# Kernel optimization log

Measured on AMD Instinct MI355X. Metric: run time of the kernel, lower is better.

## Reference

```python
import jax, jax.numpy as jnp
import numpy as np

DIM = 384
NUM_HEADS = 12
WS = 8            # window_size
SS = 4            # shift_size
HEAD_DIM = DIM // NUM_HEADS
SCALE = HEAD_DIM ** -0.5
N = WS * WS       # tokens per window
EPS = 1e-5
MLP_HIDDEN = 4 * DIM

# relative position index (static, matches torch buffer construction)
_coords = np.stack(np.meshgrid(np.arange(WS), np.arange(WS), indexing='ij')).reshape(2, -1)
_rel = (_coords[:, :, None] - _coords[:, None, :]).transpose(1, 2, 0)  # [N,N,2]
_rel[..., 0] += WS - 1
_rel[..., 1] += WS - 1
_rel[..., 0] *= 2 * WS - 1
RPI = jnp.asarray(_rel.sum(-1))  # [N,N] int


def layer_norm(x, g, b):
    m = x.mean(-1, keepdims=True)
    v = ((x - m) ** 2).mean(-1, keepdims=True)
    return (x - m) / jnp.sqrt(v + EPS) * g + b


def window_partition(x):
    B, Hh, Ww, C = x.shape
    x = x.reshape(B, Hh // WS, WS, Ww // WS, WS, C).transpose(0, 1, 3, 2, 4, 5)
    return x.reshape(-1, WS, WS, C)


def window_reverse(w, Hh, Ww):
    B = w.shape[0] // ((Hh // WS) * (Ww // WS))
    x = w.reshape(B, Hh // WS, Ww // WS, WS, WS, -1).transpose(0, 1, 3, 2, 4, 5)
    return x.reshape(B, Hh, Ww, -1)


def attention_mask(Hp, Wp):
    # region id along each axis: 0 = [0, Hp-WS), 1 = [Hp-WS, Hp-SS), 2 = [Hp-SS, Hp)
    h_id = np.zeros(Hp, np.int32); h_id[Hp - WS:Hp - SS] = 1; h_id[Hp - SS:] = 2
    w_id = np.zeros(Wp, np.int32); w_id[Wp - WS:Wp - SS] = 1; w_id[Wp - SS:] = 2
    cnt = h_id[:, None] * 3 + w_id[None, :]                      # [Hp, Wp]
    img = jnp.asarray(cnt, jnp.float32).reshape(1, Hp, Wp, 1)
    mw = window_partition(img).reshape(-1, N)                    # [nW, N]
    am = mw[:, None, :] - mw[:, :, None]                         # [nW, N, N]
    return jnp.where(am != 0, jnp.float32(-100.0), jnp.float32(0.0))


def setup_inputs() -> dict:
    key = jax.random.key(0)
    ks = jax.random.split(key, 8)
    B, H, W = 32, 64, 64
    std = 0.02
    return {
        'x': jax.random.normal(ks[0], (B, H * W, DIM), jnp.float32),
        'qkv_w': jax.random.normal(ks[1], (DIM, 3 * DIM), jnp.float32) * std,
        'qkv_b': jnp.zeros((3 * DIM,), jnp.float32),
        'proj_w': jax.random.normal(ks[2], (DIM, DIM), jnp.float32) * std,
        'proj_b': jnp.zeros((DIM,), jnp.float32),
        'rpb_table': jax.random.normal(ks[3], ((2 * WS - 1) * (2 * WS - 1), NUM_HEADS), jnp.float32) * std,
        'n1_g': jnp.ones((DIM,), jnp.float32), 'n1_b': jnp.zeros((DIM,), jnp.float32),
        'n2_g': jnp.ones((DIM,), jnp.float32), 'n2_b': jnp.zeros((DIM,), jnp.float32),
        'fc1_w': jax.random.normal(ks[4], (DIM, MLP_HIDDEN), jnp.float32) * std,
        'fc1_b': jnp.zeros((MLP_HIDDEN,), jnp.float32),
        'fc2_w': jax.random.normal(ks[5], (MLP_HIDDEN, DIM), jnp.float32) * std,
        'fc2_b': jnp.zeros((DIM,), jnp.float32),
        'H': 64, 'W': 64,
    }


def reference(x, qkv_w, qkv_b, proj_w, proj_b, rpb_table, n1_g, n1_b, n2_g, n2_b,
              fc1_w, fc1_b, fc2_w, fc2_b, H, W):
    B, L, C = x.shape
    shortcut = x
    h = layer_norm(x, n1_g, n1_b).reshape(B, H, W, C)
    pad_r = (WS - W % WS) % WS
    pad_b = (WS - H % WS) % WS
    if pad_r or pad_b:
        h = jnp.pad(h, ((0, 0), (0, pad_b), (0, pad_r), (0, 0)))
    Hp, Wp = H + pad_b, W + pad_r
    shifted = jnp.roll(h, shift=(-SS, -SS), axis=(1, 2))
    xw = window_partition(shifted).reshape(-1, N, C)             # [B_, N, C]
    B_ = xw.shape[0]

    qkv = (xw @ qkv_w + qkv_b).reshape(B_, N, 3, NUM_HEADS, HEAD_DIM)
    q = qkv[:, :, 0].transpose(0, 2, 1, 3) * SCALE               # [B_, h, N, d]
    k = qkv[:, :, 1].transpose(0, 2, 1, 3)
    v = qkv[:, :, 2].transpose(0, 2, 1, 3)

    attn = jnp.einsum('bhnd,bhmd->bhnm', q, k)                   # [B_, h, N, N]
    bias = rpb_table[RPI].transpose(2, 0, 1)                     # [h, N, N]
    attn = attn + bias[None]

    mask = attention_mask(Hp, Wp)                                # [nW, N, N]
    nW = mask.shape[0]
    attn = attn.reshape(B_ // nW, nW, NUM_HEADS, N, N) + mask[None, :, None]
    attn = jax.nn.softmax(attn.reshape(B_, NUM_HEADS, N, N), axis=-1)

    out = jnp.einsum('bhnm,bhmd->bhnd', attn, v)
    out = out.transpose(0, 2, 1, 3).reshape(B_, N, C)
    out = out @ proj_w + proj_b

    out = window_reverse(out.reshape(-1, WS, WS, C), Hp, Wp)
    out = jnp.roll(out, shift=(SS, SS), axis=(1, 2))
    out = out[:, :H, :W, :].reshape(B, H * W, C)

    x = shortcut + out
    h2 = layer_norm(x, n2_g, n2_b)
    mlp = jax.nn.gelu(h2 @ fc1_w + fc1_b, approximate=False) @ fc2_w + fc2_b
    return x + mlp
```

## Files before the change

### kernel.cpp

```cpp
#include <hip/hip_runtime.h>
#include <math.h>


#define ROWS_TOTAL 131072
#define NWIN_TOTAL 2048

typedef __attribute__((ext_vector_type(8))) __bf16 bf16x8;
typedef __attribute__((ext_vector_type(4))) float f32x4;
typedef __attribute__((ext_vector_type(8))) unsigned short ushort8;

__device__ __forceinline__ unsigned short f2bf(float f) {
  unsigned u = __builtin_bit_cast(unsigned, f);
  u = (u + 0x7fffu + ((u >> 16) & 1u)) >> 16;
  return (unsigned short)u;
}
__device__ __forceinline__ float bf2f(unsigned short u) {
  return __builtin_bit_cast(float, (unsigned)u << 16);
}

__device__ __forceinline__ void gload16(const void* g, void* l) {
  __builtin_amdgcn_global_load_lds(
      (const __attribute__((address_space(1))) unsigned int*)g,
      (__attribute__((address_space(3))) unsigned int*)l, 16, 0, 0);
}

__device__ __forceinline__ int gather_row(int win, int t) {
  int b = win >> 6, wi = (win >> 3) & 7, wj = win & 7;
  int gi = (wi * 8 + (t >> 3) + 4) & 63;
  int gj = (wj * 8 + (t & 7) + 4) & 63;
  return (b << 12) + (gi << 6) + gj;
}

__device__ __forceinline__ float gelu_f(float v) {
  float x = v * 0.70710678118654752f;
  float ax = fabsf(x);
  float t = 1.f / (1.f + 0.3275911f * ax);
  float poly =
      t * (0.254829592f +
           t * (-0.284496736f +
                t * (1.421413741f + t * (-1.453152027f + t * 1.061405429f))));
  float er = 1.f - poly * __expf(-x * x);
  er = copysignf(er, x);
  return 0.5f * v * (1.f + er);
}

#define STG(buf_, t_)                                                   \
  {                                                                     \
    size_t ko = (size_t)(t_) * 64;                                      \
    gload16(aS0 + ko, (char*)As + (buf_) * 8192 + tid * 16);            \
    gload16(aS1 + ko, (char*)As + (buf_) * 8192 + 4096 + tid * 16);     \
    gload16(bS0 + ko, (char*)Bs + (buf_) * 6144 + tid * 16);            \
    if (tid < 128)                                                      \
      gload16(bS1 + ko, (char*)Bs + (buf_) * 6144 + 4096 + tid * 16);   \
  }

#define GEMM_DECLS()                                                    \
  f32x4 acc[4][3];                                                      \
  _Pragma("unroll") for (int i_ = 0; i_ < 4; ++i_)                      \
  _Pragma("unroll") for (int j_ = 0; j_ < 3; ++j_)                      \
      acc[i_][j_] = (f32x4)(0.f);                                       \
  int aO[4], bO[3];                                                     \
  _Pragma("unroll") for (int mi_ = 0; mi_ < 4; ++mi_)                   \
      aO[mi_] = (wr * 64 + mi_ * 16 + lr) * 32 + hi * 8;                \
  _Pragma("unroll") for (int nj_ = 0; nj_ < 3; ++nj_)                   \
      bO[nj_] = (wc * 48 + nj_ * 16 + lr) * 32 + hi * 8;

#define GEMM_CORE(NT_)                                                  \
  {                                                                     \
    int cur = 0;                                                        \
    STG(0, 0);                                                          \
    __syncthreads();                                                    \
    for (int t = 0; t < (NT_); ++t) {                                   \
      if (t + 1 < (NT_)) STG(cur ^ 1, t + 1);                           \
      const ushort* AsC = &As[cur][0];                                  \
      const ushort* BsC = &Bs[cur][0];                                  \
      bf16x8 bv[3];                                                     \
      _Pragma("unroll") for (int nj = 0; nj < 3; ++nj)                  \
          bv[nj] = *(const bf16x8*)(BsC + bO[nj]);                      \
      _Pragma("unroll") for (int mi = 0; mi < 4; ++mi) {                \
        bf16x8 av = *(const bf16x8*)(AsC + aO[mi]);                     \
        _Pragma("unroll") for (int nj = 0; nj < 3; ++nj)                \
          acc[mi][nj] = __builtin_amdgcn_mfma_f32_16x16x32_bf16(        \
              av, bv[nj], acc[mi][nj], 0, 0, 0);                        \
      }                                                                 \
      __syncthreads();                                                  \
      cur ^= 1;                                                         \
    }                                                                   \
  }

#define GRID_SWZ(NP_)                                                   \
  int p, bm;                                                            \
  {                                                                     \
    int lin = blockIdx.y * (NP_) + blockIdx.x;                          \
    if ((gridDim.y & 7) == 0) {                                         \
      int xcd = lin & 7, q = lin >> 3;                                  \
      p = q % (NP_); bm = (q / (NP_)) * 8 + xcd;                        \
    } else { p = blockIdx.x; bm = blockIdx.y; }                         \
  }

__global__ __launch_bounds__(256) void wprep_k(
    const float* __restrict__ qkvw, const float* __restrict__ projw,
    const float* __restrict__ fc1w, const float* __restrict__ fc2w,
    ushort* __restrict__ wq, ushort* __restrict__ wp,
    ushort* __restrict__ w1, ushort* __restrict__ w2) {
  int gid = blockIdx.x * 256 + threadIdx.x;
  const int S1 = 1152 * 384;
  const int S2 = S1 + 384 * 384;
  const int S3 = S2 + 1536 * 384;
  const int S4 = S3 + 384 * 1536;
  if (gid < S1) {
    int n = gid / 384, k = gid - n * 384;
    wq[gid] = f2bf(qkvw[(size_t)k * 1152 + n]);
  } else if (gid < S2) {
    int i = gid - S1, n = i / 384, k = i - n * 384;
    wp[i] = f2bf(projw[(size_t)k * 384 + n]);
  } else if (gid < S3) {
    int i = gid - S2, n = i / 384, k = i - n * 384;
    w1[i] = f2bf(fc1w[(size_t)k * 1536 + n]);
  } else if (gid < S4) {
    int i = gid - S3, n = i / 1536, k = i - n * 1536;
    w2[i] = f2bf(fc2w[(size_t)k * 384 + n]);
  }
}

__global__ __launch_bounds__(256) void ln_fused_k(
    const float* __restrict__ x, const float* __restrict__ g,
    const float* __restrict__ b, ushort* __restrict__ o) {
  int wid = threadIdx.x >> 6, lane = threadIdx.x & 63;
  int row = (blockIdx.x << 2) + wid;
  const float* p = x + (size_t)row * 384;
  float2 v[3];
  float s = 0.f, ss = 0.f;
#pragma unroll
  for (int c = 0; c < 3; ++c) {
    v[c] = *(const float2*)(p + lane * 2 + c * 128);
    s += v[c].x + v[c].y;
    ss += v[c].x * v[c].x + v[c].y * v[c].y;
  }
#pragma unroll
  for (int off = 1; off < 64; off <<= 1) {
    s += __shfl_xor(s, off);
    ss += __shfl_xor(ss, off);
  }
  float m = s * (1.f / 384.f);
  float r = rsqrtf(ss * (1.f / 384.f) - m * m + 1e-5f);
  ushort* op = o + (size_t)row * 384;
#pragma unroll
  for (int c = 0; c < 3; ++c) {
    float2 gg = *(const float2*)(g + lane * 2 + c * 128);
    float2 bb = *(const float2*)(b + lane * 2 + c * 128);
    union { ushort u[2]; unsigned w; } pk;
    pk.u[0] = f2bf((v[c].x - m) * r * gg.x + bb.x);
    pk.u[1] = f2bf((v[c].y - m) * r * gg.y + bb.y);
    *(unsigned*)(op + lane * 2 + c * 128) = pk.w;
  }
}

__global__ __launch_bounds__(256) void qkv_mfma_k(
    const ushort* __restrict__ xln, const ushort* __restrict__ wq,
    const float* __restrict__ qkvb, ushort* __restrict__ qkvd, int wc0) {
  __shared__ __align__(16) ushort As[2][4096];
  __shared__ __align__(16) ushort Bs[2][3072];
  const int tid = threadIdx.x;
  const int lane = tid & 63;
  const int w = tid >> 6;
  const int wr = w >> 1, wc = w & 1;
  const int lr = lane & 15, hi = lane >> 4;
  GRID_SWZ(12);
  const int n0 = p * 96;
  int r0 = tid >> 2, r1 = (256 + tid) >> 2;
  const char* aS0 = (const char*)xln +
                    (size_t)gather_row(wc0 + bm * 2 + (r0 >> 6), r0 & 63) * 768 +
                    (tid & 3) * 16;
  const char* aS1 = (const char*)xln +
                    (size_t)gather_row(wc0 + bm * 2 + (r1 >> 6), r1 & 63) * 768 +
                    ((256 + tid) & 3) * 16;
  const char* bS0 = (const char*)wq + (size_t)(n0 + (tid >> 2)) * 768 +
                    (tid & 3) * 16;
  const char* bS1 = (const char*)wq + (size_t)(n0 + 64 + (tid >> 2)) * 768 +
                    (tid & 3) * 16;
  GEMM_DECLS();
  GEMM_CORE(12);
  const float scale = 0.17677669529663687f;
#pragma unroll
  for (int mi = 0; mi < 4; ++mi) {
#pragma unroll
    for (int r = 0; r < 4; ++r) {
      int rr = wr * 64 + mi * 16 + (hi << 2) + r;
      size_t row = (size_t)(bm * 128 + rr);
#pragma unroll
      for (int nj = 0; nj < 3; ++nj) {
        int nc = n0 + wc * 48 + nj * 16 + lr;
        float v = acc[mi][nj][r] + qkvb[nc];
        if (nc < 384) v *= scale;
        qkvd[row * 1152 + nc] = f2bf(v);
      }
    }
  }
}

__global__ __launch_bounds__(128) void attn_k(
    const ushort* __restrict__ qkv, const float* __restrict__ rpb,
    ushort* __restrict__ ao, int wc0) {
  __shared__ __align__(16) float kbuf[2][64][32];
  __shared__ __align__(16) float vbuf[2][64][32];
  __shared__ float bias[2][232];
  __shared__ int region[64];
  const int tid = threadIdx.x;
  const int wid = tid >> 6, lane = tid & 63;
  const int w = blockIdx.x, win = wc0 + w;
  const int head = blockIdx.y * 2 + wid;
  if (tid < 64) {
    int wi = (win >> 3) & 7, wj = win & 7;
    int pi = wi * 8 + (tid >> 3), pj = wj * 8 + (tid & 7);
    int ri = pi < 56 ? 0 : (pi < 60 ? 1 : 2);
    int rj = pj < 56 ? 0 : (pj < 60 ? 1 : 2);
    region[tid] = ri * 3 + rj;
  }
  const ushort* base = qkv + (size_t)(w * 64) * 1152;
  const int kcol = 384 + head * 32, vcol = 768 + head * 32;
#pragma unroll
  for (int s = 0; s < 4; ++s) {
    int f = s * 64 + lane;
    int r = f >> 2, c = (f & 3) * 8;
    ushort8 ku = *(const ushort8*)(base + (size_t)r * 1152 + kcol + c);
    ushort8 vu = *(const ushort8*)(base + (size_t)r * 1152 + vcol + c);
#pragma unroll
    for (int j = 0; j < 8; ++j) {
      kbuf[wid][r][c + j] = bf2f(ku[j]);
      vbuf[wid][r][c + j] = bf2f(vu[j]);
    }
  }
  for (int s = lane; s < 225; s += 64) bias[wid][s] = rpb[s * 12 + head];
  __syncthreads();
  const int i = lane;
  float qr[32];
  const ushort* qp = base + (size_t)i * 1152 + head * 32;
#pragma unroll
  for (int c = 0; c < 4; ++c) {
    ushort8 qu = *(const ushort8*)(qp + c * 8);
#pragma unroll
    for (int j = 0; j < 8; ++j) qr[c * 8 + j] = bf2f(qu[j]);
  }
  const int yi = i >> 3, xi = i & 7, regi = region[i];
  float sc[64];
  float mx = -3.0e38f;
#pragma unroll
  for (int j = 0; j < 64; ++j) {
    float a = 0.f;
#pragma unroll
    for (int c = 0; c < 32; c += 4) {
      float4 kv = *(float4*)&kbuf[wid][j][c];
      a = fmaf(qr[c], kv.x, a);
      a = fmaf(qr[c + 1], kv.y, a);
      a = fmaf(qr[c + 2], kv.z, a);
      a = fmaf(qr[c + 3], kv.w, a);
    }
    int dy = yi - (j >> 3) + 7, dx = xi - (j & 7) + 7;
    a += bias[wid][dy * 15 + dx];
    if (region[j] != regi) a -= 100.f;
    sc[j] = a;
    mx = fmaxf(mx, a);
  }
  float sum = 0.f;
#pragma unroll
  for (int j = 0; j < 64; ++j) {
    float e = __expf(sc[j] - mx);
    sc[j] = e;
    sum += e;
  }
  const float inv = 1.f / sum;
  float o[32];
#pragma unroll
  for (int c = 0; c < 32; ++c) o[c] = 0.f;
#pragma unroll
  for (int j = 0; j < 64; ++j) {
    float p = sc[j];
#pragma unroll
    for (int c = 0; c < 32; c += 4) {
      float4 vv = *(float4*)&vbuf[wid][j][c];
      o[c] = fmaf(p, vv.x, o[c]);
      o[c + 1] = fmaf(p, vv.y, o[c + 1]);
      o[c + 2] = fmaf(p, vv.z, o[c + 2]);
      o[c + 3] = fmaf(p, vv.w, o[c + 3]);
    }
  }
  ushort* op = ao + ((size_t)(w * 64 + i)) * 384 + (head << 5);
#pragma unroll
  for (int c = 0; c < 32; c += 8) {
    ushort8 pk;
#pragma unroll
    for (int j2 = 0; j2 < 8; ++j2) pk[j2] = f2bf(o[c + j2] * inv);
    *(ushort8*)(op + c) = pk;
  }
}

__global__ __launch_bounds__(256) void proj_mfma_k(
    const ushort* __restrict__ ao, const ushort* __restrict__ wp,
    const float* __restrict__ pb, const float* __restrict__ x,
    float* __restrict__ x2, int wc0) {
  __shared__ __align__(16) ushort As[2][4096];
  __shared__ __align__(16) ushort Bs[2][3072];
  const int tid = threadIdx.x;
  const int lane = tid & 63;
  const int w = tid >> 6;
  const int wr = w >> 1, wc = w & 1;
  const int lr = lane & 15, hi = lane >> 4;
  GRID_SWZ(4);
  const int n0 = p * 96;
  const char* aS0 = (const char*)ao +
                    (size_t)(bm * 128 + (tid >> 2)) * 768 + (tid & 3) * 16;
  const char* aS1 = (const char*)ao +
                    (size_t)(bm * 128 + 64 + (tid >> 2)) * 768 + (tid & 3) * 16;
  const char* bS0 = (const char*)wp + (size_t)(n0 + (tid >> 2)) * 768 +
                    (tid & 3) * 16;
  const char* bS1 = (const char*)wp + (size_t)(n0 + 64 + (tid >> 2)) * 768 +
                    (tid & 3) * 16;
  GEMM_DECLS();
  GEMM_CORE(12);
#pragma unroll
  for (int mi = 0; mi < 4; ++mi) {
#pragma unroll
    for (int r = 0; r < 4; ++r) {
      int rr = wr * 64 + mi * 16 + (hi << 2) + r;
      int gl = bm * 128 + rr;
      int gr = gather_row(wc0 + (gl >> 6), gl & 63);
#pragma unroll
      for (int nj = 0; nj < 3; ++nj) {
        int nc = n0 + wc * 48 + nj * 16 + lr;
        size_t idx = (size_t)gr * 384 + nc;
        x2[idx] = acc[mi][nj][r] + pb[nc] + x[idx];
      }
    }
  }
}

__global__ __launch_bounds__(256) void fc1_mfma_k(
    const ushort* __restrict__ x2ln, const ushort* __restrict__ w1,
    const float* __restrict__ fb, ushort* __restrict__ hm, int row0) {
  __shared__ __align__(16) ushort As[2][4096];
  __shared__ __align__(16) ushort Bs[2][3072];
  const int tid = threadIdx.x;
  const int lane = tid & 63;
  const int w = tid >> 6;
  const int wr = w >> 1, wc = w & 1;
  const int lr = lane & 15, hi = lane >> 4;
  GRID_SWZ(16);
  const int n0 = p * 96;
  const char* aS0 = (const char*)x2ln +
                    (size_t)(row0 + bm * 128 + (tid >> 2)) * 768 +
                    (tid & 3) * 16;
  const char* aS1 = (const char*)x2ln +
                    (size_t)(row0 + bm * 128 + 64 + (tid >> 2)) * 768 +
                    (tid & 3) * 16;
  const char* bS0 = (const char*)w1 + (size_t)(n0 + (tid >> 2)) * 768 +
                    (tid & 3) * 16;
  const char* bS1 = (const char*)w1 + (size_t)(n0 + 64 + (tid >> 2)) * 768 +
                    (tid & 3) * 16;
  GEMM_DECLS();
  GEMM_CORE(12);
#pragma unroll
  for (int mi = 0; mi < 4; ++mi) {
#pragma unroll
    for (int r = 0; r < 4; ++r) {
      int rr = wr * 64 + mi * 16 + (hi << 2) + r;
      size_t lrow = (size_t)(bm * 128 + rr);
#pragma unroll
      for (int nj = 0; nj < 3; ++nj) {
        int nc = n0 + wc * 48 + nj * 16 + lr;
        float v = gelu_f(acc[mi][nj][r] + fb[nc]);
        hm[lrow * 1536 + nc] = f2bf(v);
      }
    }
  }
}

__global__ __launch_bounds__(256) void fc2_mfma_k(
    const ushort* __restrict__ hm, const ushort* __restrict__ w2,
    const float* __restrict__ fb, float* __restrict__ out, int row0) {
  __shared__ __align__(16) ushort As[2][4096];
  __shared__ __align__(16) ushort Bs[2][3072];
  const int tid = threadIdx.x;
  const int lane = tid & 63;
  const int w = tid >> 6;
  const int wr = w >> 1, wc = w & 1;
  const int lr = lane & 15, hi = lane >> 4;
  GRID_SWZ(4);
  const int n0 = p * 96;
  const char* aS0 = (const char*)hm +
                    (size_t)(bm * 128 + (tid >> 2)) * 3072 + (tid & 3) * 16;
  const char* aS1 = (const char*)hm +
                    (size_t)(bm * 128 + 64 + (tid >> 2)) * 3072 +
                    (tid & 3) * 16;
  const char* bS0 = (const char*)w2 + (size_t)(n0 + (tid >> 2)) * 3072 +
                    (tid & 3) * 16;
  const char* bS1 = (const char*)w2 + (size_t)(n0 + 64 + (tid >> 2)) * 3072 +
                    (tid & 3) * 16;
  GEMM_DECLS();
  GEMM_CORE(48);
#pragma unroll
  for (int mi = 0; mi < 4; ++mi) {
#pragma unroll
    for (int r = 0; r < 4; ++r) {
      int rr = wr * 64 + mi * 16 + (hi << 2) + r;
      size_t grow = (size_t)(row0 + bm * 128 + rr);
#pragma unroll
      for (int nj = 0; nj < 3; ++nj) {
        int nc = n0 + wc * 48 + nj * 16 + lr;
        size_t idx = grow * 384 + nc;
        out[idx] = out[idx] + acc[mi][nj][r] + fb[nc];
      }
    }
  }
}

extern "C" void kernel_launch(void* const* d_in, const int* in_sizes, int n_in,
                              void* d_out, int out_size, void* d_ws, size_t ws_size,
                              hipStream_t stream) {
  const float* x = (const float*)d_in[0];
  const float* qkv_w = (const float*)d_in[1];
  const float* qkv_b = (const float*)d_in[2];
  const float* proj_w = (const float*)d_in[3];
  const float* proj_b = (const float*)d_in[4];
  const float* rpb = (const float*)d_in[5];
  const float* n1g = (const float*)d_in[6];
  const float* n1b = (const float*)d_in[7];
  const float* n2g = (const float*)d_in[8];
  const float* n2b = (const float*)d_in[9];
  const float* fc1w = (const float*)d_in[10];
  const float* fc1b = (const float*)d_in[11];
  const float* fc2w = (const float*)d_in[12];
  const float* fc2b = (const float*)d_in[13];
  float* out = (float*)d_out;
  char* ws = (char*)d_ws;

  ushort* wq = (ushort*)ws;
  ushort* wp = wq + 442368;
  ushort* w1 = wp + 147456;
  ushort* w2 = w1 + 589824;
  ushort* xln = (ushort*)(ws + 3538944);
  char* scratch = ws + 3538944 + 100663296;
  size_t base = 3538944 + 100663296;
  size_t ssz = (ws_size > base) ? ws_size - base : 0;

  wprep_k<<<6912, 256, 0, stream>>>(qkv_w, proj_w, fc1w, fc2w, wq, wp, w1, w2);
  ln_fused_k<<<ROWS_TOTAL / 4, 256, 0, stream>>>(x, n1g, n1b, xln);

  const size_t perwin = 196608;
  int nwc = (int)(ssz / perwin);
  if (nwc > NWIN_TOTAL) nwc = NWIN_TOTAL;
  nwc &= ~31;
  if (nwc < 32) nwc = 32;
  ushort* qkvd = (ushort*)scratch;
  ushort* ao = qkvd + (size_t)nwc * 73728;
  for (int wc0 = 0; wc0 < NWIN_TOTAL; wc0 += nwc) {
    int nw = (NWIN_TOTAL - wc0 < nwc) ? (NWIN_TOTAL - wc0) : nwc;
    qkv_mfma_k<<<dim3(12, nw / 2), 256, 0, stream>>>(xln, wq, qkv_b, qkvd,
                                                     wc0);
    attn_k<<<dim3(nw, 6), 128, 0, stream>>>(qkvd, rpb, ao, wc0);
    proj_mfma_k<<<dim3(4, nw / 2), 256, 0, stream>>>(ao, wp, proj_b, x, out,
                                                     wc0);
  }

  ln_fused_k<<<ROWS_TOTAL / 4, 256, 0, stream>>>(out, n2g, n2b, xln);
  const size_t pergrp = 393216;
  int ngc = (int)(ssz / pergrp);
  if (ngc > 1024) ngc = 1024;
  ngc &= ~7;
  if (ngc < 8) ngc = 8;
  ushort* hm = (ushort*)scratch;
  for (int g0 = 0; g0 < 1024; g0 += ngc) {
    int ng = (1024 - g0 < ngc) ? (1024 - g0) : ngc;
    fc1_mfma_k<<<dim3(16, ng), 256, 0, stream>>>(xln, w1, fc1b, hm, g0 * 128);
    fc2_mfma_k<<<dim3(4, ng), 256, 0, stream>>>(hm, w2, fc2b, out, g0 * 128);
  }
}
```

Measured before the change: 1.548 ms.

## Swizzle GEMM LDS tiles and store Q/K/V in per-head contiguous layout

Adds an XOR-style rotation of the 16-byte chunk positions, applied both to the global source offsets of the direct-to-LDS loads and to the LDS read offsets in all MFMA GEMMs. The goal is to remove LDS bank conflicts on the bf16x8 fragment reads. Separately, the QKV GEMM epilogue now writes Q, K and V into separate per-window, per-head contiguous buffers. This lets the attention kernel read its K/V/Q rows with contiguous 64-byte accesses instead of strided 2304-byte rows. The cost is scattered, less coalesced stores in the QKV epilogue.

Measured after the change: 1.552 ms. Within noise of the previous version (+0.2%).

```diff
diff --git a/kernel.cpp b/kernel.cpp
--- a/kernel.cpp
+++ b/kernel.cpp
@@ -60,10 +60,14 @@
   _Pragma("unroll") for (int j_ = 0; j_ < 3; ++j_)                      \
       acc[i_][j_] = (f32x4)(0.f);                                       \
   int aO[4], bO[3];                                                     \
-  _Pragma("unroll") for (int mi_ = 0; mi_ < 4; ++mi_)                   \
-      aO[mi_] = (wr * 64 + mi_ * 16 + lr) * 32 + hi * 8;                \
-  _Pragma("unroll") for (int nj_ = 0; nj_ < 3; ++nj_)                   \
-      bO[nj_] = (wc * 48 + nj_ * 16 + lr) * 32 + hi * 8;
+  _Pragma("unroll") for (int mi_ = 0; mi_ < 4; ++mi_) {                 \
+    int row_ = wr * 64 + mi_ * 16 + lr;                                 \
+    aO[mi_] = row_ * 32 + (((hi + (row_ >> 1)) & 3) << 3);              \
+  }                                                                     \
+  _Pragma("unroll") for (int nj_ = 0; nj_ < 3; ++nj_) {                 \
+    int row_ = wc * 48 + nj_ * 16 + lr;                                 \
+    bO[nj_] = row_ * 32 + (((hi + (row_ >> 1)) & 3) << 3);              \
+  }
 
 #define GEMM_CORE(NT_)                                                  \
   {                                                                     \
@@ -97,6 +101,8 @@
       p = q % (NP_); bm = (q / (NP_)) * 8 + xcd;                        \
     } else { p = blockIdx.x; bm = blockIdx.y; }                         \
   }
+
+#define SRC_SWZ(t_) (((((t_) & 3) - (((t_) >> 3) & 3)) & 3) << 4)
 
 __global__ __launch_bounds__(256) void wprep_k(
     const float* __restrict__ qkvw, const float* __restrict__ projw,
@@ -158,7 +164,8 @@
 
 __global__ __launch_bounds__(256) void qkv_mfma_k(
     const ushort* __restrict__ xln, const ushort* __restrict__ wq,
-    const float* __restrict__ qkvb, ushort* __restrict__ qkvd, int wc0) {
+    const float* __restrict__ qkvb, ushort* __restrict__ qd,
+    ushort* __restrict__ kd, ushort* __restrict__ vd, int wc0) {
   __shared__ __align__(16) ushort As[2][4096];
   __shared__ __align__(16) ushort Bs[2][3072];
   const int tid = threadIdx.x;
@@ -171,14 +178,14 @@
   int r0 = tid >> 2, r1 = (256 + tid) >> 2;
   const char* aS0 = (const char*)xln +
                     (size_t)gather_row(wc0 + bm * 2 + (r0 >> 6), r0 & 63) * 768 +
-                    (tid & 3) * 16;
+                    SRC_SWZ(tid);
   const char* aS1 = (const char*)xln +
                     (size_t)gather_row(wc0 + bm * 2 + (r1 >> 6), r1 & 63) * 768 +
-                    ((256 + tid) & 3) * 16;
+                    SRC_SWZ(tid);
   const char* bS0 = (const char*)wq + (size_t)(n0 + (tid >> 2)) * 768 +
-                    (tid & 3) * 16;
+                    SRC_SWZ(tid);
   const char* bS1 = (const char*)wq + (size_t)(n0 + 64 + (tid >> 2)) * 768 +
-                    (tid & 3) * 16;
+                    SRC_SWZ(tid);
   GEMM_DECLS();
   GEMM_CORE(12);
   const float scale = 0.17677669529663687f;
@@ -187,20 +194,24 @@
 #pragma unroll
     for (int r = 0; r < 4; ++r) {
       int rr = wr * 64 + mi * 16 + (hi << 2) + r;
-      size_t row = (size_t)(bm * 128 + rr);
+      int w_rel = bm * 2 + (rr >> 6), t = rr & 63;
 #pragma unroll
       for (int nj = 0; nj < 3; ++nj) {
         int nc = n0 + wc * 48 + nj * 16 + lr;
         float v = acc[mi][nj][r] + qkvb[nc];
-        if (nc < 384) v *= scale;
-        qkvd[row * 1152 + nc] = f2bf(v);
+        int qi = nc / 384, rem = nc - qi * 384;
+        int hh = rem >> 5, d = rem & 31;
+        ushort* base = (qi == 0) ? qd : (qi == 1 ? kd : vd);
+        if (qi == 0) v *= scale;
+        base[(((size_t)w_rel * 12 + hh) << 11) + (t << 5) + d] = f2bf(v);
       }
     }
   }
 }
 
 __global__ __launch_bounds__(128) void attn_k(
-    const ushort* __restrict__ qkv, const float* __restrict__ rpb,
+    const ushort* __restrict__ q, const ushort* __restrict__ k,
+    const ushort* __restrict__ v, const float* __restrict__ rpb,
     ushort* __restrict__ ao, int wc0) {
   __shared__ __align__(16) float kbuf[2][64][32];
   __shared__ __align__(16) float vbuf[2][64][32];
@@ -217,14 +228,15 @@
     int rj = pj < 56 ? 0 : (pj < 60 ? 1 : 2);
     region[tid] = ri * 3 + rj;
   }
-  const ushort* base = qkv + (size_t)(w * 64) * 1152;
-  const int kcol = 384 + head * 32, vcol = 768 + head * 32;
+  const size_t hb = ((size_t)w * 12 + head) * 2048;
+  const ushort* kp = k + hb;
+  const ushort* vp = v + hb;
 #pragma unroll
   for (int s = 0; s < 4; ++s) {
     int f = s * 64 + lane;
     int r = f >> 2, c = (f & 3) * 8;
-    ushort8 ku = *(const ushort8*)(base + (size_t)r * 1152 + kcol + c);
-    ushort8 vu = *(const ushort8*)(base + (size_t)r * 1152 + vcol + c);
+    ushort8 ku = *(const ushort8*)(kp + r * 32 + c);
+    ushort8 vu = *(const ushort8*)(vp + r * 32 + c);
 #pragma unroll
     for (int j = 0; j < 8; ++j) {
       kbuf[wid][r][c + j] = bf2f(ku[j]);
@@ -235,7 +247,7 @@
   __syncthreads();
   const int i = lane;
   float qr[32];
-  const ushort* qp = base + (size_t)i * 1152 + head * 32;
+  const ushort* qp = q + hb + (i << 5);
 #pragma unroll
   for (int c = 0; c < 4; ++c) {
     ushort8 qu = *(const ushort8*)(qp + c * 8);
@@ -309,13 +321,13 @@
   GRID_SWZ(4);
   const int n0 = p * 96;
   const char* aS0 = (const char*)ao +
-                    (size_t)(bm * 128 + (tid >> 2)) * 768 + (tid & 3) * 16;
+                    (size_t)(bm * 128 + (tid >> 2)) * 768 + SRC_SWZ(tid);
   const char* aS1 = (const char*)ao +
-                    (size_t)(bm * 128 + 64 + (tid >> 2)) * 768 + (tid & 3) * 16;
+                    (size_t)(bm * 128 + 64 + (tid >> 2)) * 768 + SRC_SWZ(tid);
   const char* bS0 = (const char*)wp + (size_t)(n0 + (tid >> 2)) * 768 +
-                    (tid & 3) * 16;
+                    SRC_SWZ(tid);
   const char* bS1 = (const char*)wp + (size_t)(n0 + 64 + (tid >> 2)) * 768 +
-                    (tid & 3) * 16;
+                    SRC_SWZ(tid);
   GEMM_DECLS();
   GEMM_CORE(12);
 #pragma unroll
@@ -349,14 +361,14 @@
   const int n0 = p * 96;
   const char* aS0 = (const char*)x2ln +
                     (size_t)(row0 + bm * 128 + (tid >> 2)) * 768 +
-                    (tid & 3) * 16;
+                    SRC_SWZ(tid);
   const char* aS1 = (const char*)x2ln +
                     (size_t)(row0 + bm * 128 + 64 + (tid >> 2)) * 768 +
-                    (tid & 3) * 16;
+                    SRC_SWZ(tid);
   const char* bS0 = (const char*)w1 + (size_t)(n0 + (tid >> 2)) * 768 +
-                    (tid & 3) * 16;
+                    SRC_SWZ(tid);
   const char* bS1 = (const char*)w1 + (size_t)(n0 + 64 + (tid >> 2)) * 768 +
-                    (tid & 3) * 16;
+                    SRC_SWZ(tid);
   GEMM_DECLS();
   GEMM_CORE(12);
 #pragma unroll
@@ -388,14 +400,14 @@
   GRID_SWZ(4);
   const int n0 = p * 96;
   const char* aS0 = (const char*)hm +
-                    (size_t)(bm * 128 + (tid >> 2)) * 3072 + (tid & 3) * 16;
+                    (size_t)(bm * 128 + (tid >> 2)) * 3072 + SRC_SWZ(tid);
   const char* aS1 = (const char*)hm +
                     (size_t)(bm * 128 + 64 + (tid >> 2)) * 3072 +
-                    (tid & 3) * 16;
+                    SRC_SWZ(tid);
   const char* bS0 = (const char*)w2 + (size_t)(n0 + (tid >> 2)) * 3072 +
-                    (tid & 3) * 16;
+                    SRC_SWZ(tid);
   const char* bS1 = (const char*)w2 + (size_t)(n0 + 64 + (tid >> 2)) * 3072 +
-                    (tid & 3) * 16;
+                    SRC_SWZ(tid);
   GEMM_DECLS();
   GEMM_CORE(48);
 #pragma unroll
@@ -451,13 +463,15 @@
   if (nwc > NWIN_TOTAL) nwc = NWIN_TOTAL;
   nwc &= ~31;
   if (nwc < 32) nwc = 32;
-  ushort* qkvd = (ushort*)scratch;
-  ushort* ao = qkvd + (size_t)nwc * 73728;
+  ushort* qd = (ushort*)scratch;
+  ushort* kd = qd + (size_t)nwc * 24576;
+  ushort* vd = kd + (size_t)nwc * 24576;
+  ushort* ao = vd + (size_t)nwc * 24576;
   for (int wc0 = 0; wc0 < NWIN_TOTAL; wc0 += nwc) {
     int nw = (NWIN_TOTAL - wc0 < nwc) ? (NWIN_TOTAL - wc0) : nwc;
-    qkv_mfma_k<<<dim3(12, nw / 2), 256, 0, stream>>>(xln, wq, qkv_b, qkvd,
-                                                     wc0);
-    attn_k<<<dim3(nw, 6), 128, 0, stream>>>(qkvd, rpb, ao, wc0);
+    qkv_mfma_k<<<dim3(12, nw / 2), 256, 0, stream>>>(xln, wq, qkv_b, qd, kd,
+                                                     vd, wc0);
+    attn_k<<<dim3(nw, 6), 128, 0, stream>>>(qd, kd, vd, rpb, ao, wc0);
     proj_mfma_k<<<dim3(4, nw / 2), 256, 0, stream>>>(ao, wp, proj_b, x, out,
                                                      wc0);
   }
```
